# Kernel optimization log

Measured on AMD Instinct MI355X. Metric: run time of the kernel, lower is better.

## Reference

```python
import jax, jax.numpy as jnp
import numpy as np

T = 2048      # query tokens
S = 2048      # kv tokens
H = 16        # heads
DN = 128      # qk_nope_head_dim
DR = 64       # qk_rope_head_dim
DV = 128      # v_head_dim
CLR = 512     # kv_lora_rank
DIM = 2048    # model dim
SCALE = 1.0 / np.sqrt(DN + DR)
NEG = -1e30


def setup_inputs() -> dict:
    key = jax.random.key(0)
    ks = jax.random.split(key, 6)
    return {
        "q_nope": jax.random.normal(ks[0], (T, H, DN), jnp.float32) * 0.05,
        "q_pe": jax.random.normal(ks[1], (T, H, DR), jnp.float32) * 0.05,
        "kv_all": jax.random.normal(ks[2], (S, CLR), jnp.float32) * 0.05,
        "pe_all": jax.random.normal(ks[3], (S, DR), jnp.float32) * 0.05,
        "wkv_b": jax.random.normal(ks[4], (H, DN + DV, CLR), jnp.float32) * 0.02,
        "wo": jax.random.normal(ks[5], (DIM, H * DV), jnp.float32) * 0.02,
        "prompt_cache_len": 0,
    }


def reference(q_nope, q_pe, kv_all, pe_all, wkv_b, wo, prompt_cache_len):
    # Decompress latent KV per head: wkv_b[:, :DN] -> k_nope weights, wkv_b[:, -DV:] -> v weights
    w_k = wkv_b[:, :DN, :]            # [H, DN, C]
    w_v = wkv_b[:, -DV:, :]           # [H, DV, C]
    k_nope = jnp.einsum('sc,hdc->shd', kv_all, w_k)   # [S, H, DN]
    v = jnp.einsum('sc,hdc->shd', kv_all, w_v)        # [S, H, DV]
    # Combined nope + rope logits
    logits = (jnp.einsum('thd,shd->ths', q_nope, k_nope)
              + jnp.einsum('thd,sd->ths', q_pe, pe_all)) * SCALE  # [T, H, S]
    # Causal mask with prompt-cache offset
    q_pos = jnp.arange(T) + prompt_cache_len
    k_pos = jnp.arange(S)
    mask = k_pos[None, :] <= q_pos[:, None]           # [T, S]
    logits = jnp.where(mask[:, None, :], logits, NEG)
    attn = jax.nn.softmax(logits, axis=-1)
    out_v = jnp.einsum('ths,shd->thd', attn, v)       # [T, H, DV]
    return out_v.reshape(T, H * DV) @ wo.T            # [T, DIM]
```

## Files before the change

kernel.cpp:

```cpp
#include <hip/hip_runtime.h>

#define T_ 2048
#define S_ 2048
#define H_ 16
#define DQK 192
#define DV_ 128
#define CLR_ 512
#define DIM_ 2048
#define SCALE_ 0.07216878364870322f

typedef unsigned short u16;
typedef unsigned int u32;
typedef __attribute__((ext_vector_type(8))) u16 u16x8;
typedef __attribute__((ext_vector_type(4))) u16 u16x4;
typedef __attribute__((ext_vector_type(8))) __bf16 bf16x8;
typedef __attribute__((ext_vector_type(4))) float f32x4;

__device__ __forceinline__ u16 f2bf(float f) {
  u32 x = __builtin_bit_cast(u32, f);
  u32 r = x + 0x7fffu + ((x >> 16) & 1u);
  return (u16)(r >> 16);
}

__device__ __forceinline__ f32x4 mfma16(u16x8 a, u16x8 b, f32x4 c) {
  return __builtin_amdgcn_mfma_f32_16x16x32_bf16(
      __builtin_bit_cast(bf16x8, a), __builtin_bit_cast(bf16x8, b), c, 0, 0, 0);
}

__device__ __forceinline__ void gload16(const u16* g, const u16* lds_base) {
  auto gp = reinterpret_cast<const __attribute__((address_space(1))) unsigned int*>(
      reinterpret_cast<uintptr_t>(g));
  auto lp = reinterpret_cast<__attribute__((address_space(3))) unsigned int*>(
      reinterpret_cast<uintptr_t>(lds_base));
  __builtin_amdgcn_global_load_lds(gp, lp, 16, 0, 0);
}

__global__ __launch_bounds__(256) void k_build(
    const float* __restrict__ qn, const float* __restrict__ qp,
    const float* __restrict__ pe, const float* __restrict__ kv,
    const float* __restrict__ wkv, const float* __restrict__ wo,
    u16* __restrict__ Qc, u16* __restrict__ Kc,
    u16* __restrict__ kvb, u16* __restrict__ wkvb, u16* __restrict__ wob) {
  u32 gid = blockIdx.x * 256u + threadIdx.x;
  u32 stride = gridDim.x * 256u;

  const u32 NQ = H_ * T_ * 48u;
  for (u32 i = gid; i < NQ; i += stride) {
    u32 j4 = i % 48u;
    u32 th = i / 48u;
    u32 t = th & (T_ - 1);
    u32 h = th >> 11;
    float4 v = (j4 < 32u) ? *(const float4*)(qn + ((size_t)t * H_ + h) * 128 + j4 * 4)
                          : *(const float4*)(qp + ((size_t)t * H_ + h) * 64 + (j4 - 32u) * 4);
    u16x4 o = {f2bf(v.x), f2bf(v.y), f2bf(v.z), f2bf(v.w)};
    *(u16x4*)(Qc + (size_t)th * DQK + j4 * 4) = o;
  }
  const u32 NP = H_ * S_ * 16u;
  for (u32 i = gid; i < NP; i += stride) {
    u32 j4 = i & 15u;
    u32 s = (i >> 4) & (S_ - 1);
    u32 h = i >> 15;
    float4 v = *(const float4*)(pe + (size_t)s * 64 + j4 * 4);
    u16x4 o = {f2bf(v.x), f2bf(v.y), f2bf(v.z), f2bf(v.w)};
    *(u16x4*)(Kc + ((size_t)h * S_ + s) * DQK + 128 + j4 * 4) = o;
  }
  const u32 NKV = (2048u * 512u) / 4u;
  for (u32 i = gid; i < NKV; i += stride) {
    float4 v = *(const float4*)(kv + (size_t)i * 4);
    u16x4 o = {f2bf(v.x), f2bf(v.y), f2bf(v.z), f2bf(v.w)};
    *(u16x4*)(kvb + (size_t)i * 4) = o;
  }
  const u32 NW = (4096u * 512u) / 4u;
  for (u32 i = gid; i < NW; i += stride) {
    float4 v = *(const float4*)(wkv + (size_t)i * 4);
    u16x4 o = {f2bf(v.x), f2bf(v.y), f2bf(v.z), f2bf(v.w)};
    *(u16x4*)(wkvb + (size_t)i * 4) = o;
  }
  const u32 NO = (2048u * 2048u) / 4u;
  for (u32 i = gid; i < NO; i += stride) {
    float4 v = *(const float4*)(wo + (size_t)i * 4);
    u16x4 o = {f2bf(v.x), f2bf(v.y), f2bf(v.z), f2bf(v.w)};
    *(u16x4*)(wob + (size_t)i * 4) = o;
  }
}

__global__ __launch_bounds__(256) void k_expand(
    const u16* __restrict__ kvb, const u16* __restrict__ wkvb,
    u16* __restrict__ Kc, u16* __restrict__ Vt) {
  __shared__ __align__(16) u16 Al[2 * 128 * 64];
  __shared__ __align__(16) u16 Bl[2 * 128 * 64];
  int tid = threadIdx.x;
  int wave = tid >> 6, lane = tid & 63, lr = lane & 15, lq = lane >> 4;
  int wm = wave >> 1, wn = wave & 1;
  int s0 = blockIdx.x * 128, n0 = blockIdx.y * 128;
  f32x4 acc[4][4] = {};

  auto stage = [&](int buf, int kc) {
#pragma unroll
    for (int i = 0; i < 4; ++i) {
      int ch = tid + 256 * i;
      int r = ch >> 3, c8 = (ch & 7) * 8;
      const u16* lbA = Al + buf * 8192 + wave * 512 + i * 2048;
      const u16* lbB = Bl + buf * 8192 + wave * 512 + i * 2048;
      gload16(kvb + (size_t)(s0 + r) * CLR_ + kc + c8, lbA);
      gload16(wkvb + (size_t)(n0 + r) * CLR_ + kc + c8, lbB);
    }
  };

  stage(0, 0);
  __syncthreads();
  int buf = 0;
  const int nt = CLR_ / 64;
  for (int t = 0; t < nt; ++t) {
    if (t + 1 < nt) stage(buf ^ 1, (t + 1) * 64);
#pragma unroll
    for (int ks = 0; ks < 2; ++ks) {
      u16x8 a[4], b[4];
#pragma unroll
      for (int m = 0; m < 4; ++m)
        a[m] = *(const u16x8*)&Al[buf * 8192 + (wm * 64 + m * 16 + lr) * 64 + ks * 32 + lq * 8];
#pragma unroll
      for (int n = 0; n < 4; ++n)
        b[n] = *(const u16x8*)&Bl[buf * 8192 + (wn * 64 + n * 16 + lr) * 64 + ks * 32 + lq * 8];
#pragma unroll
      for (int m = 0; m < 4; ++m)
#pragma unroll
        for (int n = 0; n < 4; ++n) acc[m][n] = mfma16(a[m], b[n], acc[m][n]);
    }
    __syncthreads();
    buf ^= 1;
  }
#pragma unroll
  for (int m = 0; m < 4; ++m) {
    int s = s0 + wm * 64 + m * 16 + lq * 4;
#pragma unroll
    for (int n = 0; n < 4; ++n) {
      int nn = n0 + wn * 64 + n * 16 + lr;
      int h = nn >> 8, cc = nn & 255;
#pragma unroll
      for (int r = 0; r < 4; ++r) {
        u16 bv = f2bf(acc[m][n][r]);
        if (cc < 128) Kc[((size_t)h * S_ + s + r) * DQK + cc] = bv;
        else          Vt[((size_t)h * 128 + (cc - 128)) * S_ + s + r] = bv;
      }
    }
  }
}

__global__ __launch_bounds__(512, 4) void k_attn(
    const u16* __restrict__ Qc, const u16* __restrict__ Kc,
    const u16* __restrict__ Vt, u16* __restrict__ Ob,
    const int* __restrict__ pclp) {
  __shared__ __align__(16) u16 Kl[2][64][200];
  __shared__ __align__(16) u16 Pl[8][16][40];
  int h = blockIdx.y;
  int qt = ((h >> 3) & 1) ? (int)blockIdx.x : (int)(31 - blockIdx.x);
  int t0 = qt * 64;
  int pcl = *pclp;
  int tid = threadIdx.x;
  int wave = tid >> 6, lane = tid & 63, lr = lane & 15, lq = lane >> 4;
  int g = wave & 3, ep = wave >> 2;

  u16x8 qf[6];
  const u16* qb = Qc + ((size_t)h * T_ + t0 + g * 16 + lr) * DQK;
#pragma unroll
  for (int k = 0; k < 6; ++k) qf[k] = *(const u16x8*)(qb + k * 32 + lq * 8);

  f32x4 acc[8] = {};
  float dsum[4] = {0.f, 0.f, 0.f, 0.f};

  long smax = (long)t0 + 63 + (long)pcl;
  if (smax > (long)(S_ - 1)) smax = S_ - 1;
  int np = (int)(smax >> 6) + 1;

  const u16* kc_base = Kc + (size_t)h * S_ * DQK;
  const u16* vb = Vt + (size_t)h * 128 * S_ + (size_t)lr * S_ + lq * 8;
  int tg = t0 + g * 16 + lq * 4 + pcl;

  u16x8 gk[3];
#pragma unroll
  for (int i = 0; i < 3; ++i) {
    int ch = tid + 512 * i;
    int r = ch / 24, c = ch % 24;
    gk[i] = *(const u16x8*)(kc_base + (size_t)r * DQK + c * 8);
  }
#pragma unroll
  for (int i = 0; i < 3; ++i) {
    int ch = tid + 512 * i;
    int r = ch / 24, c = ch % 24;
    *(u16x8*)&Kl[0][r][c * 8] = gk[i];
  }
  __syncthreads();

  int buf = 0;
  for (int p = 0; p < np; ++p) {
    int sp0 = p * 64;
    bool more = (p + 1 < np);
    if (more) {
#pragma unroll
      for (int i = 0; i < 3; ++i) {
        int ch = tid + 512 * i;
        int r = ch / 24, c = ch % 24;
        gk[i] = *(const u16x8*)(kc_base + (size_t)(sp0 + 64 + r) * DQK + c * 8);
      }
    }
    int s0v = sp0 + ep * 32;

    f32x4 lg[2] = {};
#pragma unroll
    for (int ks = 0; ks < 6; ++ks) {
#pragma unroll
      for (int nf = 0; nf < 2; ++nf) {
        u16x8 b = *(const u16x8*)&Kl[buf][ep * 32 + nf * 16 + lr][ks * 32 + lq * 8];
        lg[nf] = mfma16(qf[ks], b, lg[nf]);
      }
    }

#pragma unroll
    for (int nf = 0; nf < 2; ++nf) {
      int sg = s0v + nf * 16 + lr;
#pragma unroll
      for (int r = 0; r < 4; ++r) {
        float e = __expf(lg[nf][r] * SCALE_);
        float pv = (sg <= tg + r) ? e : 0.f;
        dsum[r] += pv;
        Pl[wave][lq * 4 + r][nf * 16 + lr] = f2bf(pv);
      }
    }
    asm volatile("s_waitcnt lgkmcnt(0)" ::: "memory");
    __builtin_amdgcn_sched_barrier(0);
    u16x8 pa = *(const u16x8*)&Pl[wave][lr][lq * 8];

#pragma unroll
    for (int db = 0; db < 8; ++db) {
      u16x8 v = *(const u16x8*)(vb + (size_t)(db * 16) * S_ + s0v);
      acc[db] = mfma16(pa, v, acc[db]);
    }

    if (more) {
#pragma unroll
      for (int i = 0; i < 3; ++i) {
        int ch = tid + 512 * i;
        int r = ch / 24, c = ch % 24;
        *(u16x8*)&Kl[buf ^ 1][r][c * 8] = gk[i];
      }
    }
    __syncthreads();
    buf ^= 1;
  }

  float* comb = (float*)&Kl[0][0][0];
  if (ep == 1) {
    float* dst = comb + (size_t)(g * 64 + lane) * 36;
#pragma unroll
    for (int db = 0; db < 8; ++db) *(f32x4*)(dst + db * 4) = acc[db];
#pragma unroll
    for (int r = 0; r < 4; ++r) dst[32 + r] = dsum[r];
  }
  __syncthreads();
  if (ep == 0) {
    const float* src = comb + (size_t)(g * 64 + lane) * 36;
#pragma unroll
    for (int db = 0; db < 8; ++db) acc[db] += *(const f32x4*)(src + db * 4);
#pragma unroll
    for (int r = 0; r < 4; ++r) dsum[r] += src[32 + r];
#pragma unroll
    for (int r = 0; r < 4; ++r) {
      float s = dsum[r];
#pragma unroll
      for (int m = 1; m < 16; m <<= 1) s += __shfl_xor(s, m, 64);
      float inv = 1.f / s;
      int t = t0 + g * 16 + lq * 4 + r;
#pragma unroll
      for (int db = 0; db < 8; ++db)
        Ob[(size_t)t * (H_ * DV_) + h * DV_ + db * 16 + lr] = f2bf(acc[db][r] * inv);
    }
  }
}

__global__ __launch_bounds__(256) void k_proj(
    const u16* __restrict__ A, const u16* __restrict__ wob,
    float* __restrict__ out) {
  __shared__ __align__(16) u16 Al[2 * 64 * 64];
  __shared__ __align__(16) u16 Bl[2 * 128 * 64];
  int tid = threadIdx.x;
  int wave = tid >> 6, lane = tid & 63, lr = lane & 15, lq = lane >> 4;
  int wm = wave >> 1, wn = wave & 1;
  int t0 = blockIdx.x * 64, o0 = blockIdx.y * 128;
  f32x4 acc[2][4] = {};

  auto stage = [&](int buf, int kc) {
#pragma unroll
    for (int i = 0; i < 2; ++i) {
      int ch = tid + 256 * i;
      int r = ch >> 3, c8 = (ch & 7) * 8;
      const u16* lbA = Al + buf * 4096 + wave * 512 + i * 2048;
      gload16(A + (size_t)(t0 + r) * DIM_ + kc + c8, lbA);
    }
#pragma unroll
    for (int i = 0; i < 4; ++i) {
      int ch = tid + 256 * i;
      int r = ch >> 3, c8 = (ch & 7) * 8;
      const u16* lbB = Bl + buf * 8192 + wave * 512 + i * 2048;
      gload16(wob + (size_t)(o0 + r) * DIM_ + kc + c8, lbB);
    }
  };

  stage(0, 0);
  __syncthreads();
  int buf = 0;
  const int nt = DIM_ / 64;
  for (int t = 0; t < nt; ++t) {
    if (t + 1 < nt) stage(buf ^ 1, (t + 1) * 64);
#pragma unroll
    for (int ks = 0; ks < 2; ++ks) {
      u16x8 a[2], b[4];
#pragma unroll
      for (int m = 0; m < 2; ++m)
        a[m] = *(const u16x8*)&Al[buf * 4096 + (wm * 32 + m * 16 + lr) * 64 + ks * 32 + lq * 8];
#pragma unroll
      for (int n = 0; n < 4; ++n)
        b[n] = *(const u16x8*)&Bl[buf * 8192 + (wn * 64 + n * 16 + lr) * 64 + ks * 32 + lq * 8];
#pragma unroll
      for (int m = 0; m < 2; ++m)
#pragma unroll
        for (int n = 0; n < 4; ++n) acc[m][n] = mfma16(a[m], b[n], acc[m][n]);
    }
    __syncthreads();
    buf ^= 1;
  }
#pragma unroll
  for (int m = 0; m < 2; ++m) {
    int t = t0 + wm * 32 + m * 16 + lq * 4;
#pragma unroll
    for (int n = 0; n < 4; ++n) {
      int o = o0 + wn * 64 + n * 16 + lr;
#pragma unroll
      for (int r = 0; r < 4; ++r)
        out[(size_t)(t + r) * DIM_ + o] = acc[m][n][r];
    }
  }
}

extern "C" void kernel_launch(void* const* d_in, const int* in_sizes, int n_in,
                              void* d_out, int out_size, void* d_ws, size_t ws_size,
                              hipStream_t stream) {
  const float* qn  = (const float*)d_in[0];
  const float* qp  = (const float*)d_in[1];
  const float* kv  = (const float*)d_in[2];
  const float* pe  = (const float*)d_in[3];
  const float* wkv = (const float*)d_in[4];
  const float* wo  = (const float*)d_in[5];
  const int*   pcl = (const int*)d_in[6];
  float* out = (float*)d_out;

  char* ws = (char*)d_ws;
  u16* Qc   = (u16*)(ws);
  u16* Kc   = (u16*)(ws + 12582912);
  u16* Vt   = (u16*)(ws + 25165824);
  u16* Ob   = (u16*)(ws + 33554432);
  u16* kvb  = (u16*)(ws + 41943040);
  u16* wkvb = (u16*)(ws + 44040192);
  u16* wob  = (u16*)(ws + 48234496);

  k_build<<<2048, 256, 0, stream>>>(qn, qp, pe, kv, wkv, wo, Qc, Kc, kvb, wkvb, wob);
  k_expand<<<dim3(16, 32), 256, 0, stream>>>(kvb, wkvb, Kc, Vt);
  k_attn<<<dim3(32, 16), 512, 0, stream>>>(Qc, Kc, Vt, Ob, pcl);
  k_proj<<<dim3(32, 16), 256, 0, stream>>>(Ob, wob, out);
}
```

Before: 278.7 us.

## Split attention over KV halves with atomic accumulation, swizzle LDS, async K loads

The attention kernel now splits the KV range into two chunks across a third grid dimension. Each 256-thread block accumulates unnormalized outputs and denominators into fp32 buffers with atomicAdd, and a new k_norm kernel then normalizes them to bf16. K tiles are staged with direct global-to-LDS loads into an XOR-swizzled layout, and V fragments are prefetched earlier in each iteration. The expand and projection GEMMs also get XOR-swizzled LDS layouts to reduce bank conflicts. In exchange it adds fp32 zeroing of the accumulation buffers, atomic traffic, and an extra launch.

```diff
diff --git a/kernel.cpp b/kernel.cpp
--- a/kernel.cpp
+++ b/kernel.cpp
@@ -40,7 +40,8 @@
     const float* __restrict__ pe, const float* __restrict__ kv,
     const float* __restrict__ wkv, const float* __restrict__ wo,
     u16* __restrict__ Qc, u16* __restrict__ Kc,
-    u16* __restrict__ kvb, u16* __restrict__ wkvb, u16* __restrict__ wob) {
+    u16* __restrict__ kvb, u16* __restrict__ wkvb, u16* __restrict__ wob,
+    float* __restrict__ O, float* __restrict__ D) {
   u32 gid = blockIdx.x * 256u + threadIdx.x;
   u32 stride = gridDim.x * 256u;
 
@@ -82,6 +83,11 @@
     u16x4 o = {f2bf(v.x), f2bf(v.y), f2bf(v.z), f2bf(v.w)};
     *(u16x4*)(wob + (size_t)i * 4) = o;
   }
+  float4 z = {0.f, 0.f, 0.f, 0.f};
+  const u32 NZ = (2048u * 2048u) / 4u;
+  for (u32 i = gid; i < NZ; i += stride) *(float4*)(O + (size_t)i * 4) = z;
+  const u32 ND = (2048u * 16u) / 4u;
+  for (u32 i = gid; i < ND; i += stride) *(float4*)(D + (size_t)i * 4) = z;
 }
 
 __global__ __launch_bounds__(256) void k_expand(
@@ -99,11 +105,12 @@
 #pragma unroll
     for (int i = 0; i < 4; ++i) {
       int ch = tid + 256 * i;
-      int r = ch >> 3, c8 = (ch & 7) * 8;
+      int r = ch >> 3;
+      int cs = ((ch & 7) ^ (r & 7)) * 8;
       const u16* lbA = Al + buf * 8192 + wave * 512 + i * 2048;
       const u16* lbB = Bl + buf * 8192 + wave * 512 + i * 2048;
-      gload16(kvb + (size_t)(s0 + r) * CLR_ + kc + c8, lbA);
-      gload16(wkvb + (size_t)(n0 + r) * CLR_ + kc + c8, lbB);
+      gload16(kvb + (size_t)(s0 + r) * CLR_ + kc + cs, lbA);
+      gload16(wkvb + (size_t)(n0 + r) * CLR_ + kc + cs, lbB);
     }
   };
 
@@ -117,11 +124,17 @@
     for (int ks = 0; ks < 2; ++ks) {
       u16x8 a[4], b[4];
 #pragma unroll
-      for (int m = 0; m < 4; ++m)
-        a[m] = *(const u16x8*)&Al[buf * 8192 + (wm * 64 + m * 16 + lr) * 64 + ks * 32 + lq * 8];
-#pragma unroll
-      for (int n = 0; n < 4; ++n)
-        b[n] = *(const u16x8*)&Bl[buf * 8192 + (wn * 64 + n * 16 + lr) * 64 + ks * 32 + lq * 8];
+      for (int m = 0; m < 4; ++m) {
+        int row = wm * 64 + m * 16 + lr;
+        int col = ((4 * ks + lq) ^ (row & 7)) * 8;
+        a[m] = *(const u16x8*)&Al[buf * 8192 + row * 64 + col];
+      }
+#pragma unroll
+      for (int n = 0; n < 4; ++n) {
+        int row = wn * 64 + n * 16 + lr;
+        int col = ((4 * ks + lq) ^ (row & 7)) * 8;
+        b[n] = *(const u16x8*)&Bl[buf * 8192 + row * 64 + col];
+      }
 #pragma unroll
       for (int m = 0; m < 4; ++m)
 #pragma unroll
@@ -147,78 +160,89 @@
   }
 }
 
-__global__ __launch_bounds__(512, 4) void k_attn(
+__global__ __launch_bounds__(256, 4) void k_attn(
     const u16* __restrict__ Qc, const u16* __restrict__ Kc,
-    const u16* __restrict__ Vt, u16* __restrict__ Ob,
-    const int* __restrict__ pclp) {
-  __shared__ __align__(16) u16 Kl[2][64][200];
-  __shared__ __align__(16) u16 Pl[8][16][40];
+    const u16* __restrict__ Vt, float* __restrict__ O,
+    float* __restrict__ D, const int* __restrict__ pclp) {
+  __shared__ __align__(16) u16 Kl[2][32 * 192];
+  __shared__ __align__(16) u16 Pl[4][16][40];
   int h = blockIdx.y;
-  int qt = ((h >> 3) & 1) ? (int)blockIdx.x : (int)(31 - blockIdx.x);
+  int qt = blockIdx.x;
+  int sc = blockIdx.z;
+  int pcl = *pclp;
   int t0 = qt * 64;
-  int pcl = *pclp;
+
+  long smax_l = (long)t0 + 63 + (long)pcl;
+  if (smax_l > (long)(S_ - 1)) smax_l = S_ - 1;
+  int smax = (int)smax_l;
+  int sbeg = sc * 1024;
+  if (sbeg > smax) return;
+  int send = sbeg + 1023 < smax ? sbeg + 1023 : smax;
+  int np = ((send - sbeg) >> 5) + 1;
+
   int tid = threadIdx.x;
   int wave = tid >> 6, lane = tid & 63, lr = lane & 15, lq = lane >> 4;
-  int g = wave & 3, ep = wave >> 2;
+
+  const u16* kc_base = Kc + (size_t)h * S_ * DQK;
+  const u16* vb = Vt + (size_t)h * 128 * S_ + (size_t)lr * S_ + lq * 8;
+  int tg = t0 + wave * 16 + lq * 4 + pcl;
+
+  int ch0 = tid, ch1 = tid + 256, ch2 = tid + 512;
+  int r0 = ch0 / 24, c0 = ch0 % 24;
+  int r1 = ch1 / 24, c1 = ch1 % 24;
+  int r2 = ch2 / 24, c2 = ch2 % 24;
+  int o0 = r0 * DQK + ((((c0 & 7) ^ (r0 & 7)) | (c0 & 24)) * 8);
+  int o1 = r1 * DQK + ((((c1 & 7) ^ (r1 & 7)) | (c1 & 24)) * 8);
+  int o2 = r2 * DQK + ((((c2 & 7) ^ (r2 & 7)) | (c2 & 24)) * 8);
+
+  auto stageK = [&](int buf, int sbase) {
+    const u16* src = kc_base + (size_t)sbase * DQK;
+    const u16* lb = &Kl[buf][0] + wave * 512;
+    gload16(src + o0, lb);
+    gload16(src + o1, lb + 2048);
+    gload16(src + o2, lb + 4096);
+  };
 
   u16x8 qf[6];
-  const u16* qb = Qc + ((size_t)h * T_ + t0 + g * 16 + lr) * DQK;
+  const u16* qb = Qc + ((size_t)h * T_ + t0 + wave * 16 + lr) * DQK;
 #pragma unroll
   for (int k = 0; k < 6; ++k) qf[k] = *(const u16x8*)(qb + k * 32 + lq * 8);
 
   f32x4 acc[8] = {};
   float dsum[4] = {0.f, 0.f, 0.f, 0.f};
 
-  long smax = (long)t0 + 63 + (long)pcl;
-  if (smax > (long)(S_ - 1)) smax = S_ - 1;
-  int np = (int)(smax >> 6) + 1;
-
-  const u16* kc_base = Kc + (size_t)h * S_ * DQK;
-  const u16* vb = Vt + (size_t)h * 128 * S_ + (size_t)lr * S_ + lq * 8;
-  int tg = t0 + g * 16 + lq * 4 + pcl;
-
-  u16x8 gk[3];
-#pragma unroll
-  for (int i = 0; i < 3; ++i) {
-    int ch = tid + 512 * i;
-    int r = ch / 24, c = ch % 24;
-    gk[i] = *(const u16x8*)(kc_base + (size_t)r * DQK + c * 8);
-  }
-#pragma unroll
-  for (int i = 0; i < 3; ++i) {
-    int ch = tid + 512 * i;
-    int r = ch / 24, c = ch % 24;
-    *(u16x8*)&Kl[0][r][c * 8] = gk[i];
-  }
+  stageK(0, sbeg);
+  asm volatile("s_waitcnt vmcnt(0)" ::: "memory");
   __syncthreads();
 
   int buf = 0;
   for (int p = 0; p < np; ++p) {
-    int sp0 = p * 64;
+    int s0 = sbeg + p * 32;
     bool more = (p + 1 < np);
-    if (more) {
-#pragma unroll
-      for (int i = 0; i < 3; ++i) {
-        int ch = tid + 512 * i;
-        int r = ch / 24, c = ch % 24;
-        gk[i] = *(const u16x8*)(kc_base + (size_t)(sp0 + 64 + r) * DQK + c * 8);
-      }
-    }
-    int s0v = sp0 + ep * 32;
+
+    u16x8 vfr[8];
+#pragma unroll
+    for (int db = 0; db < 8; ++db)
+      vfr[db] = *(const u16x8*)(vb + (size_t)(db * 16) * S_ + s0);
+
+    if (more) stageK(buf ^ 1, s0 + 32);
 
     f32x4 lg[2] = {};
 #pragma unroll
     for (int ks = 0; ks < 6; ++ks) {
 #pragma unroll
       for (int nf = 0; nf < 2; ++nf) {
-        u16x8 b = *(const u16x8*)&Kl[buf][ep * 32 + nf * 16 + lr][ks * 32 + lq * 8];
+        int row = nf * 16 + lr;
+        int c16 = 4 * ks + lq;
+        int col = (((c16 & 7) ^ (row & 7)) | (c16 & 24)) * 8;
+        u16x8 b = *(const u16x8*)&Kl[buf][row * DQK + col];
         lg[nf] = mfma16(qf[ks], b, lg[nf]);
       }
     }
 
 #pragma unroll
     for (int nf = 0; nf < 2; ++nf) {
-      int sg = s0v + nf * 16 + lr;
+      int sg = s0 + nf * 16 + lr;
 #pragma unroll
       for (int r = 0; r < 4; ++r) {
         float e = __expf(lg[nf][r] * SCALE_);
@@ -232,50 +256,48 @@
     u16x8 pa = *(const u16x8*)&Pl[wave][lr][lq * 8];
 
 #pragma unroll
-    for (int db = 0; db < 8; ++db) {
-      u16x8 v = *(const u16x8*)(vb + (size_t)(db * 16) * S_ + s0v);
-      acc[db] = mfma16(pa, v, acc[db]);
-    }
+    for (int db = 0; db < 8; ++db) acc[db] = mfma16(pa, vfr[db], acc[db]);
 
     if (more) {
-#pragma unroll
-      for (int i = 0; i < 3; ++i) {
-        int ch = tid + 512 * i;
-        int r = ch / 24, c = ch % 24;
-        *(u16x8*)&Kl[buf ^ 1][r][c * 8] = gk[i];
-      }
-    }
-    __syncthreads();
+      asm volatile("s_waitcnt vmcnt(0)" ::: "memory");
+      __syncthreads();
+    }
     buf ^= 1;
   }
 
-  float* comb = (float*)&Kl[0][0][0];
-  if (ep == 1) {
-    float* dst = comb + (size_t)(g * 64 + lane) * 36;
-#pragma unroll
-    for (int db = 0; db < 8; ++db) *(f32x4*)(dst + db * 4) = acc[db];
-#pragma unroll
-    for (int r = 0; r < 4; ++r) dst[32 + r] = dsum[r];
-  }
-  __syncthreads();
-  if (ep == 0) {
-    const float* src = comb + (size_t)(g * 64 + lane) * 36;
-#pragma unroll
-    for (int db = 0; db < 8; ++db) acc[db] += *(const f32x4*)(src + db * 4);
-#pragma unroll
-    for (int r = 0; r < 4; ++r) dsum[r] += src[32 + r];
+#pragma unroll
+  for (int r = 0; r < 4; ++r) {
+    float s = dsum[r];
+#pragma unroll
+    for (int m = 1; m < 16; m <<= 1) s += __shfl_xor(s, m, 64);
+    if (lr == 0) {
+      int t = t0 + wave * 16 + lq * 4 + r;
+      atomicAdd(&D[t * H_ + h], s);
+    }
+  }
+#pragma unroll
+  for (int db = 0; db < 8; ++db) {
 #pragma unroll
     for (int r = 0; r < 4; ++r) {
-      float s = dsum[r];
-#pragma unroll
-      for (int m = 1; m < 16; m <<= 1) s += __shfl_xor(s, m, 64);
-      float inv = 1.f / s;
-      int t = t0 + g * 16 + lq * 4 + r;
-#pragma unroll
-      for (int db = 0; db < 8; ++db)
-        Ob[(size_t)t * (H_ * DV_) + h * DV_ + db * 16 + lr] = f2bf(acc[db][r] * inv);
-    }
-  }
+      int t = t0 + wave * 16 + lq * 4 + r;
+      atomicAdd(&O[(size_t)t * (H_ * DV_) + h * DV_ + db * 16 + lr], acc[db][r]);
+    }
+  }
+}
+
+__global__ __launch_bounds__(256) void k_norm(
+    const float* __restrict__ O, const float* __restrict__ D,
+    u16* __restrict__ Ob) {
+  u32 gid = blockIdx.x * 256u + threadIdx.x;
+  u32 j = gid * 8u;
+  u32 t = j >> 11;
+  u32 hh = (j & 2047u) >> 7;
+  float inv = 1.f / D[t * H_ + hh];
+  f32x4 v0 = *(const f32x4*)(O + j);
+  f32x4 v1 = *(const f32x4*)(O + j + 4);
+  u16x8 o = {f2bf(v0[0] * inv), f2bf(v0[1] * inv), f2bf(v0[2] * inv), f2bf(v0[3] * inv),
+             f2bf(v1[0] * inv), f2bf(v1[1] * inv), f2bf(v1[2] * inv), f2bf(v1[3] * inv)};
+  *(u16x8*)(Ob + j) = o;
 }
 
 __global__ __launch_bounds__(256) void k_proj(
@@ -293,16 +315,18 @@
 #pragma unroll
     for (int i = 0; i < 2; ++i) {
       int ch = tid + 256 * i;
-      int r = ch >> 3, c8 = (ch & 7) * 8;
+      int r = ch >> 3;
+      int cs = ((ch & 7) ^ (r & 7)) * 8;
       const u16* lbA = Al + buf * 4096 + wave * 512 + i * 2048;
-      gload16(A + (size_t)(t0 + r) * DIM_ + kc + c8, lbA);
+      gload16(A + (size_t)(t0 + r) * DIM_ + kc + cs, lbA);
     }
 #pragma unroll
     for (int i = 0; i < 4; ++i) {
       int ch = tid + 256 * i;
-      int r = ch >> 3, c8 = (ch & 7) * 8;
+      int r = ch >> 3;
+      int cs = ((ch & 7) ^ (r & 7)) * 8;
       const u16* lbB = Bl + buf * 8192 + wave * 512 + i * 2048;
-      gload16(wob + (size_t)(o0 + r) * DIM_ + kc + c8, lbB);
+      gload16(wob + (size_t)(o0 + r) * DIM_ + kc + cs, lbB);
     }
   };
 
@@ -316,11 +340,17 @@
     for (int ks = 0; ks < 2; ++ks) {
       u16x8 a[2], b[4];
 #pragma unroll
-      for (int m = 0; m < 2; ++m)
-        a[m] = *(const u16x8*)&Al[buf * 4096 + (wm * 32 + m * 16 + lr) * 64 + ks * 32 + lq * 8];
-#pragma unroll
-      for (int n = 0; n < 4; ++n)
-        b[n] = *(const u16x8*)&Bl[buf * 8192 + (wn * 64 + n * 16 + lr) * 64 + ks * 32 + lq * 8];
+      for (int m = 0; m < 2; ++m) {
+        int row = wm * 32 + m * 16 + lr;
+        int col = ((4 * ks + lq) ^ (row & 7)) * 8;
+        a[m] = *(const u16x8*)&Al[buf * 4096 + row * 64 + col];
+      }
+#pragma unroll
+      for (int n = 0; n < 4; ++n) {
+        int row = wn * 64 + n * 16 + lr;
+        int col = ((4 * ks + lq) ^ (row & 7)) * 8;
+        b[n] = *(const u16x8*)&Bl[buf * 8192 + row * 64 + col];
+      }
 #pragma unroll
       for (int m = 0; m < 2; ++m)
 #pragma unroll
@@ -355,16 +385,19 @@
   float* out = (float*)d_out;
 
   char* ws = (char*)d_ws;
-  u16* Qc   = (u16*)(ws);
-  u16* Kc   = (u16*)(ws + 12582912);
-  u16* Vt   = (u16*)(ws + 25165824);
-  u16* Ob   = (u16*)(ws + 33554432);
-  u16* kvb  = (u16*)(ws + 41943040);
-  u16* wkvb = (u16*)(ws + 44040192);
-  u16* wob  = (u16*)(ws + 48234496);
-
-  k_build<<<2048, 256, 0, stream>>>(qn, qp, pe, kv, wkv, wo, Qc, Kc, kvb, wkvb, wob);
+  u16*   Qc   = (u16*)(ws);
+  u16*   Ob   = (u16*)(ws);
+  u16*   Kc   = (u16*)(ws + 12582912);
+  u16*   Vt   = (u16*)(ws + 25165824);
+  u16*   kvb  = (u16*)(ws + 33554432);
+  u16*   wkvb = (u16*)(ws + 35651584);
+  u16*   wob  = (u16*)(ws + 39845888);
+  float* O    = (float*)(ws + 48234496);
+  float* Dd   = (float*)(ws + 65011712);
+
+  k_build<<<2048, 256, 0, stream>>>(qn, qp, pe, kv, wkv, wo, Qc, Kc, kvb, wkvb, wob, O, Dd);
   k_expand<<<dim3(16, 32), 256, 0, stream>>>(kvb, wkvb, Kc, Vt);
-  k_attn<<<dim3(32, 16), 512, 0, stream>>>(Qc, Kc, Vt, Ob, pcl);
+  k_attn<<<dim3(32, 16, 2), 256, 0, stream>>>(Qc, Kc, Vt, O, Dd, pcl);
+  k_norm<<<2048, 256, 0, stream>>>(O, Dd, Ob);
   k_proj<<<dim3(32, 16), 256, 0, stream>>>(Ob, wob, out);
 }
```

Result: slower. 301.3 us (+8.1%).
